# Optimization experiments

Measured on AMD Instinct MI355X. Metric: run time of the kernel, lower is better.

The kernel has to match this reference:

```python
import jax, jax.numpy as jnp
import numpy as np

B, N, D = 4, 2048, 1024


def setup_inputs() -> dict:
    key = jax.random.key(0)
    ks = jax.random.split(key, 9)
    x = jax.random.normal(ks[0], (B, N, D), dtype=jnp.float32)
    # causal mask: True = masked (set to -inf), per dot_product_attention semantics
    mask = jnp.triu(jnp.ones((N, N), dtype=bool), k=1)
    mask = jnp.broadcast_to(mask, (B, N, N))
    scale = 1.0 / np.sqrt(D)
    Wq = jax.random.normal(ks[1], (D, D), dtype=jnp.float32) * scale
    Wk = jax.random.normal(ks[2], (D, D), dtype=jnp.float32) * scale
    Wv = jax.random.normal(ks[3], (D, D), dtype=jnp.float32) * scale
    Wo = jax.random.normal(ks[4], (D, D), dtype=jnp.float32) * scale
    bq = jnp.zeros((D,), dtype=jnp.float32)
    bk = jnp.zeros((D,), dtype=jnp.float32)
    bv = jnp.zeros((D,), dtype=jnp.float32)
    bo = jnp.zeros((D,), dtype=jnp.float32)
    return {"x": x, "mask": mask, "Wq": Wq, "bq": bq, "Wk": Wk, "bk": bk,
            "Wv": Wv, "bv": bv, "Wo": Wo, "bo": bo}


def reference(x, mask, Wq, bq, Wk, bk, Wv, bv, Wo, bo):
    # QKV projections (single-head despite docstring; module never splits heads)
    Q = x @ Wq + bq  # [b, n, d]
    K = x @ Wk + bk
    V = x @ Wv + bv
    d = K.shape[-1]
    scores = jnp.einsum('bqd,bkd->bqk', Q, K) / jnp.sqrt(jnp.asarray(d, Q.dtype))
    min_infty = jnp.finfo(scores.dtype).min
    scores = jnp.where(mask, min_infty, scores)
    weights = jax.nn.softmax(scores, axis=-1)
    attention = jnp.einsum('bqk,bkd->bqd', weights, V)
    out = attention @ Wo + bo
    return out
```

## Files before the change

### kernel.cpp

```cpp
#include <hip/hip_runtime.h>
#include <hip/hip_bf16.h>

typedef __attribute__((ext_vector_type(8))) short short8;
typedef __attribute__((ext_vector_type(4))) float f32x4;

__device__ inline float b2f(unsigned short u) {
    union { unsigned int i; float f; } c; c.i = ((unsigned int)u) << 16; return c.f;
}
__device__ inline unsigned short f2b(float f) {
    __hip_bfloat16 h = __float2bfloat16(f);
    return *reinterpret_cast<unsigned short*>(&h);
}

__device__ inline void gl_lds16(const unsigned short* g, unsigned short* ldsbase) {
    __builtin_amdgcn_global_load_lds(
        (const __attribute__((address_space(1))) unsigned int*)(g),
        (__attribute__((address_space(3))) unsigned int*)(ldsbase),
        16, 0, 0);
}

__global__ __launch_bounds__(256) void cvt_f32_bf16(
    const float* __restrict__ src, unsigned short* __restrict__ dst, int n4)
{
    int i = blockIdx.x * 256 + threadIdx.x;
    if (i >= n4) return;
    float4 v = ((const float4*)src)[i];
    union { unsigned short u[4]; unsigned long long ll; } p;
    p.u[0] = f2b(v.x); p.u[1] = f2b(v.y); p.u[2] = f2b(v.z); p.u[3] = f2b(v.w);
    ((unsigned long long*)dst)[i] = p.ll;
}

__global__ __launch_bounds__(256) void cvt_weights4(
    const float* __restrict__ s0, const float* __restrict__ s1, const float* __restrict__ s2,
    const float* __restrict__ s3,
    unsigned short* __restrict__ d0, unsigned short* __restrict__ d1,
    unsigned short* __restrict__ d2, unsigned short* __restrict__ d3)
{
    const int z = blockIdx.z;
    if (z == 3) {
        const int i = (blockIdx.y * 32 + blockIdx.x) * 256 + threadIdx.x;
        float4 v = ((const float4*)s3)[i];
        union { unsigned short u[4]; unsigned long long ll; } p;
        p.u[0] = f2b(v.x); p.u[1] = f2b(v.y); p.u[2] = f2b(v.z); p.u[3] = f2b(v.w);
        ((unsigned long long*)d3)[i] = p.ll;
        return;
    }
    const float* src = z == 0 ? s0 : z == 1 ? s1 : s2;
    unsigned short* dst = z == 0 ? d0 : z == 1 ? d1 : d2;
    __shared__ float tile[32][33];
    const int c0 = blockIdx.x * 32, r0 = blockIdx.y * 32;
    const int tx = threadIdx.x & 31, ty = threadIdx.x >> 5;
    #pragma unroll
    for (int i = ty; i < 32; i += 8)
        tile[i][tx] = src[(long)(r0 + i) * 1024 + c0 + tx];
    __syncthreads();
    #pragma unroll
    for (int i = ty; i < 32; i += 8)
        dst[(long)(c0 + i) * 1024 + r0 + tx] = f2b(tile[tx][i]);
}

__global__ __launch_bounds__(64) void make_bvo(
    const unsigned short* __restrict__ Wot, const float* __restrict__ bv,
    const float* __restrict__ bo, float* __restrict__ bvo)
{
    const int n = blockIdx.x;
    const int lane = threadIdx.x;
    const unsigned short* row = Wot + (long)n * 1024;
    float acc = 0.f;
    #pragma unroll
    for (int pass = 0; pass < 2; pass++) {
        const int k = pass * 512 + lane * 8;
        short8 wv = *(const short8*)(row + k);
        #pragma unroll
        for (int j = 0; j < 8; j++)
            acc += bv[k + j] * b2f((unsigned short)wv[j]);
    }
    #pragma unroll
    for (int off = 32; off > 0; off >>= 1) acc += __shfl_xor(acc, off, 64);
    if (lane == 0) bvo[n] = acc + bo[n];
}

#define TILE_DECLS \
    __shared__ __attribute__((aligned(16))) unsigned short As[2 * 128 * 32]; \
    __shared__ __attribute__((aligned(16))) unsigned short Bs[2 * 128 * 32]; \
    const int t = threadIdx.x, lane = t & 63, w = t >> 6; \
    const int wr = w >> 1, wc = w & 1; \
    const int lrow = lane & 15, quad = lane >> 4; \
    f32x4 acc[4][4]; \
    _Pragma("unroll") for (int i = 0; i < 4; i++) \
        _Pragma("unroll") for (int j = 0; j < 4; j++) \
            acc[i][j] = (f32x4){0.f, 0.f, 0.f, 0.f};

#define TILE_KLOOP(gA, lda, gB, ldb, Keff) \
    for (int k0 = 0; k0 < (Keff); k0 += 64) { \
        _Pragma("unroll") for (int p = 0; p < 2; p++) \
            _Pragma("unroll") for (int h = 0; h < 2; h++) { \
                gl_lds16((gA) + (long)h * 16 * (lda) + k0 + p * 32, \
                         &As[p * 4096 + (w * 32 + h * 16) * 32]); \
                gl_lds16((gB) + (long)h * 16 * (ldb) + k0 + p * 32, \
                         &Bs[p * 4096 + (w * 32 + h * 16) * 32]); \
            } \
        __syncthreads(); \
        _Pragma("unroll") for (int p = 0; p < 2; p++) { \
            short8 af[4], bfr[4]; \
            _Pragma("unroll") for (int mi = 0; mi < 4; mi++) \
                af[mi] = *(const short8*)&As[p * 4096 + (wr * 64 + mi * 16 + lrow) * 32 + quad * 8]; \
            _Pragma("unroll") for (int ni = 0; ni < 4; ni++) \
                bfr[ni] = *(const short8*)&Bs[p * 4096 + (wc * 64 + ni * 16 + lrow) * 32 + quad * 8]; \
            _Pragma("unroll") for (int mi = 0; mi < 4; mi++) \
                _Pragma("unroll") for (int ni = 0; ni < 4; ni++) \
                    acc[mi][ni] = __builtin_amdgcn_mfma_f32_16x16x32_bf16( \
                        af[mi], bfr[ni], acc[mi][ni], 0, 0, 0); \
        } \
        __syncthreads(); \
    }

__global__ __launch_bounds__(256) void qkv_proj(
    const unsigned short* __restrict__ A,
    const unsigned short* __restrict__ Wqt, const unsigned short* __restrict__ Wkt,
    const unsigned short* __restrict__ Wvot,
    const float* __restrict__ bq, const float* __restrict__ bk,
    unsigned short* __restrict__ Q, unsigned short* __restrict__ Km,
    unsigned short* __restrict__ Vot)
{
    const int bm = blockIdx.x, bn = blockIdx.y;
    const int r = bn >> 3, bnn = bn & 7;
    const unsigned short* Bt = (r == 0) ? Wqt : (r == 1) ? Wkt : Wvot;
    const float* bias = (r == 0) ? bq : (r == 1) ? bk : nullptr;
    const int m0 = bm * 128, n0 = bnn * 128;

    TILE_DECLS

    const unsigned short* gA = A  + (long)(m0 + w * 32 + (lane >> 2)) * 1024 + (lane & 3) * 8;
    const unsigned short* gB = Bt + (long)(n0 + w * 32 + (lane >> 2)) * 1024 + (lane & 3) * 8;
    TILE_KLOOP(gA, 1024, gB, 1024, 1024)

    #pragma unroll
    for (int mi = 0; mi < 4; mi++) {
        const int m = m0 + wr * 64 + mi * 16 + quad * 4;
        #pragma unroll
        for (int ni = 0; ni < 4; ni++) {
            const int n = n0 + wc * 64 + ni * 16 + lrow;
            const float bvl = bias ? bias[n] : 0.f;
            if (r < 2) {
                unsigned short* out = (r == 0) ? Q : Km;
                #pragma unroll
                for (int rg = 0; rg < 4; rg++)
                    out[(long)(m + rg) * 1024 + n] = f2b(acc[mi][ni][rg] + bvl);
            } else {
                #pragma unroll
                for (int rg = 0; rg < 4; rg++)
                    Vot[(long)n * 8192 + m + rg] = f2b(acc[mi][ni][rg]);
            }
        }
    }
}

template<bool CAUSAL2, bool KCAUSAL, int OMODE>
__global__ __launch_bounds__(256) void gemm64(
    const unsigned short* __restrict__ A, const unsigned short* __restrict__ Bt,
    const float* __restrict__ bias, void* __restrict__ Cv,
    int K, int lda, int ldb, int ldc, long sA, long sB, long sC, float scale)
{
    const int bm = KCAUSAL ? (gridDim.x - 1 - blockIdx.x) : blockIdx.x;
    const int bn = blockIdx.y, bz = blockIdx.z;
    if (CAUSAL2 && bm < 2 * bn) return;
    A  += (long)bz * sA;
    Bt += (long)bz * sB;
    const int m0 = bm * 64, n0 = bn * 128;

    __shared__ __attribute__((aligned(16))) unsigned short As[2 * 64 * 32];
    __shared__ __attribute__((aligned(16))) unsigned short Bs[2 * 128 * 32];

    const int t = threadIdx.x, lane = t & 63, w = t >> 6;
    const int wr = w >> 1, wc = w & 1;
    const int lrow = lane & 15, quad = lane >> 4;

    f32x4 acc[2][4];
    #pragma unroll
    for (int i = 0; i < 2; i++)
        #pragma unroll
        for (int j = 0; j < 4; j++)
            acc[i][j] = (f32x4){0.f, 0.f, 0.f, 0.f};

    const int KeffRaw = KCAUSAL ? ((bm >> 1) + 1) * 128 : K;
    const int Keff = KeffRaw < K ? KeffRaw : K;

    const unsigned short* gA = A  + (long)(m0 + w * 16 + (lane >> 2)) * lda + (lane & 3) * 8;
    const unsigned short* gB = Bt + (long)(n0 + w * 32 + (lane >> 2)) * ldb + (lane & 3) * 8;

    for (int k0 = 0; k0 < Keff; k0 += 64) {
        #pragma unroll
        for (int p = 0; p < 2; p++) {
            gl_lds16(gA + k0 + p * 32, &As[p * 2048 + (w * 16) * 32]);
            gl_lds16(gB + k0 + p * 32, &Bs[p * 4096 + (w * 32) * 32]);
            gl_lds16(gB + (long)16 * ldb + k0 + p * 32, &Bs[p * 4096 + (w * 32 + 16) * 32]);
        }
        __syncthreads();
        #pragma unroll
        for (int p = 0; p < 2; p++) {
            short8 af[2], bfr[4];
            #pragma unroll
            for (int mi = 0; mi < 2; mi++)
                af[mi] = *(const short8*)&As[p * 2048 + (wr * 32 + mi * 16 + lrow) * 32 + quad * 8];
            #pragma unroll
            for (int ni = 0; ni < 4; ni++)
                bfr[ni] = *(const short8*)&Bs[p * 4096 + (wc * 64 + ni * 16 + lrow) * 32 + quad * 8];
            #pragma unroll
            for (int mi = 0; mi < 2; mi++)
                #pragma unroll
                for (int ni = 0; ni < 4; ni++)
                    acc[mi][ni] = __builtin_amdgcn_mfma_f32_16x16x32_bf16(
                        af[mi], bfr[ni], acc[mi][ni], 0, 0, 0);
        }
        __syncthreads();
    }

    #pragma unroll
    for (int mi = 0; mi < 2; mi++) {
        const int m = m0 + wr * 32 + mi * 16 + quad * 4;
        #pragma unroll
        for (int ni = 0; ni < 4; ni++) {
            const int n = n0 + wc * 64 + ni * 16 + lrow;
            const float bvl = bias ? bias[n] : 0.f;
            #pragma unroll
            for (int rg = 0; rg < 4; rg++) {
                const float val = acc[mi][ni][rg] * scale + bvl;
                if (OMODE == 1)
                    ((float*)Cv)[(long)bz * sC + (long)(m + rg) * ldc + n] = val;
                else
                    ((unsigned short*)Cv)[(long)bz * sC + (long)(m + rg) * ldc + n] = f2b(val);
            }
        }
    }
}

__global__ __launch_bounds__(256) void softmax_causal(unsigned short* __restrict__ S)
{
    const long row = blockIdx.x;
    const int i = (int)(row & 2047);
    unsigned short* base = S + row * 2048;
    const int t = threadIdx.x;
    const int padded = ((i >> 7) + 1) << 7;
    const int j0 = t * 8;
    const bool active = j0 < padded;

    __shared__ float red[4];

    float v[8];
    if (active) {
        short8 s8 = *(const short8*)(base + j0);
        #pragma unroll
        for (int jj = 0; jj < 8; jj++)
            v[jj] = (j0 + jj <= i) ? b2f((unsigned short)s8[jj]) : -3.0e38f;
    } else {
        #pragma unroll
        for (int jj = 0; jj < 8; jj++) v[jj] = -3.0e38f;
    }

    float lmax = v[0];
    #pragma unroll
    for (int jj = 1; jj < 8; jj++) lmax = fmaxf(lmax, v[jj]);
    #pragma unroll
    for (int off = 32; off > 0; off >>= 1) lmax = fmaxf(lmax, __shfl_xor(lmax, off, 64));
    if ((t & 63) == 0) red[t >> 6] = lmax;
    __syncthreads();
    const float gmax = fmaxf(fmaxf(red[0], red[1]), fmaxf(red[2], red[3]));
    __syncthreads();

    float lsum = 0.f;
    #pragma unroll
    for (int jj = 0; jj < 8; jj++) {
        v[jj] = (v[jj] > -1.0e37f) ? __expf(v[jj] - gmax) : 0.f;
        lsum += v[jj];
    }
    #pragma unroll
    for (int off = 32; off > 0; off >>= 1) lsum += __shfl_xor(lsum, off, 64);
    if ((t & 63) == 0) red[t >> 6] = lsum;
    __syncthreads();
    const float inv = 1.0f / (red[0] + red[1] + red[2] + red[3]);

    if (active) {
        short8 p8;
        #pragma unroll
        for (int jj = 0; jj < 8; jj++) p8[jj] = (short)f2b(v[jj] * inv);
        *(short8*)(base + j0) = p8;
    }
}

extern "C" void kernel_launch(void* const* d_in, const int* in_sizes, int n_in,
                              void* d_out, int out_size, void* d_ws, size_t ws_size,
                              hipStream_t stream)
{
    const float* x  = (const float*)d_in[0];
    const float* Wq = (const float*)d_in[2];
    const float* bq = (const float*)d_in[3];
    const float* Wk = (const float*)d_in[4];
    const float* bk = (const float*)d_in[5];
    const float* Wv = (const float*)d_in[6];
    const float* bv = (const float*)d_in[7];
    const float* Wo = (const float*)d_in[8];
    const float* bo = (const float*)d_in[9];

    unsigned short* ws = (unsigned short*)d_ws;
    const long XSZ = 8192L * 1024;
    const long WSZ = 1024L * 1024;
    unsigned short* xb   = ws;
    unsigned short* Wqt  = ws + XSZ;
    unsigned short* Wkt  = Wqt + WSZ;
    unsigned short* Wot  = Wkt + WSZ;
    unsigned short* Wvb  = Wot + WSZ;
    unsigned short* Wvot = Wvb + WSZ;
    unsigned short* Q    = Wvot + WSZ;
    unsigned short* Km   = Q + XSZ;
    unsigned short* Vot  = Km + XSZ;
    unsigned short* S    = Vot + XSZ;
    float*          bvo  = (float*)(S + 4L * 2048 * 2048);

    const dim3 blk(256);

    cvt_f32_bf16<<<dim3(8192), blk, 0, stream>>>(x, xb, (int)(XSZ / 4));
    cvt_weights4<<<dim3(32, 32, 4), blk, 0, stream>>>(
        Wq, Wk, Wo, Wv, Wqt, Wkt, Wot, Wvb);
    make_bvo    <<<dim3(1024), dim3(64), 0, stream>>>(Wot, bv, bo, bvo);

    gemm64<false, false, 0><<<dim3(16, 8, 1), blk, 0, stream>>>(
        Wot, Wvb, nullptr, Wvot, 1024, 1024, 1024, 1024, 0, 0, 0, 1.f);

    qkv_proj<<<dim3(64, 24), blk, 0, stream>>>(
        xb, Wqt, Wkt, Wvot, bq, bk, Q, Km, Vot);

    gemm64<true, false, 0><<<dim3(32, 16, 4), blk, 0, stream>>>(
        Q, Km, nullptr, S, 1024, 1024, 1024, 2048,
        2048L * 1024, 2048L * 1024, 2048L * 2048, 0.03125f);

    softmax_causal<<<dim3(4 * 2048), blk, 0, stream>>>(S);

    gemm64<false, true, 1><<<dim3(32, 8, 4), blk, 0, stream>>>(
        S, Vot, bvo, (float*)d_out, 2048, 2048, 8192, 1024,
        2048L * 2048, 2048, 2048L * 1024, 1.f);
}
```

Baseline: 347.6 us.

## Merge prep kernels, fuse causal QK^T with last-block softmax, retile PV to 128x128

```diff
diff --git a/kernel.cpp b/kernel.cpp
--- a/kernel.cpp
+++ b/kernel.cpp
@@ -19,65 +19,54 @@
         16, 0, 0);
 }
 
-__global__ __launch_bounds__(256) void cvt_f32_bf16(
-    const float* __restrict__ src, unsigned short* __restrict__ dst, int n4)
-{
-    int i = blockIdx.x * 256 + threadIdx.x;
-    if (i >= n4) return;
-    float4 v = ((const float4*)src)[i];
-    union { unsigned short u[4]; unsigned long long ll; } p;
-    p.u[0] = f2b(v.x); p.u[1] = f2b(v.y); p.u[2] = f2b(v.z); p.u[3] = f2b(v.w);
-    ((unsigned long long*)dst)[i] = p.ll;
-}
-
-__global__ __launch_bounds__(256) void cvt_weights4(
-    const float* __restrict__ s0, const float* __restrict__ s1, const float* __restrict__ s2,
-    const float* __restrict__ s3,
-    unsigned short* __restrict__ d0, unsigned short* __restrict__ d1,
-    unsigned short* __restrict__ d2, unsigned short* __restrict__ d3)
-{
-    const int z = blockIdx.z;
-    if (z == 3) {
-        const int i = (blockIdx.y * 32 + blockIdx.x) * 256 + threadIdx.x;
-        float4 v = ((const float4*)s3)[i];
-        union { unsigned short u[4]; unsigned long long ll; } p;
-        p.u[0] = f2b(v.x); p.u[1] = f2b(v.y); p.u[2] = f2b(v.z); p.u[3] = f2b(v.w);
-        ((unsigned long long*)d3)[i] = p.ll;
-        return;
-    }
-    const float* src = z == 0 ? s0 : z == 1 ? s1 : s2;
-    unsigned short* dst = z == 0 ? d0 : z == 1 ? d1 : d2;
-    __shared__ float tile[32][33];
-    const int c0 = blockIdx.x * 32, r0 = blockIdx.y * 32;
-    const int tx = threadIdx.x & 31, ty = threadIdx.x >> 5;
-    #pragma unroll
-    for (int i = ty; i < 32; i += 8)
-        tile[i][tx] = src[(long)(r0 + i) * 1024 + c0 + tx];
-    __syncthreads();
-    #pragma unroll
-    for (int i = ty; i < 32; i += 8)
-        dst[(long)(c0 + i) * 1024 + r0 + tx] = f2b(tile[tx][i]);
-}
-
-__global__ __launch_bounds__(64) void make_bvo(
-    const unsigned short* __restrict__ Wot, const float* __restrict__ bv,
-    const float* __restrict__ bo, float* __restrict__ bvo)
-{
-    const int n = blockIdx.x;
-    const int lane = threadIdx.x;
-    const unsigned short* row = Wot + (long)n * 1024;
-    float acc = 0.f;
-    #pragma unroll
-    for (int pass = 0; pass < 2; pass++) {
-        const int k = pass * 512 + lane * 8;
-        short8 wv = *(const short8*)(row + k);
-        #pragma unroll
-        for (int j = 0; j < 8; j++)
-            acc += bv[k + j] * b2f((unsigned short)wv[j]);
-    }
-    #pragma unroll
-    for (int off = 32; off > 0; off >>= 1) acc += __shfl_xor(acc, off, 64);
-    if (lane == 0) bvo[n] = acc + bo[n];
+__global__ __launch_bounds__(256) void prep(
+    const float* __restrict__ x, const float* __restrict__ Wq,
+    const float* __restrict__ Wk, const float* __restrict__ Wv,
+    const float* __restrict__ Wo, const float* __restrict__ bv,
+    const float* __restrict__ bo,
+    unsigned short* __restrict__ xb, unsigned short* __restrict__ Wqt,
+    unsigned short* __restrict__ Wkt, unsigned short* __restrict__ Wot,
+    unsigned short* __restrict__ Wvb, float* __restrict__ bvo,
+    unsigned int* __restrict__ tick)
+{
+    const int bid = blockIdx.x, nb = gridDim.x, t = threadIdx.x;
+    __shared__ float tile[32 * 33];
+
+    for (int j = bid; j < 3072; j += nb) {
+        const float* src = (j < 1024) ? Wq : (j < 2048) ? Wk : Wo;
+        unsigned short* dst = (j < 1024) ? Wqt : (j < 2048) ? Wkt : Wot;
+        const int ji = j & 1023;
+        const int c0 = (ji & 31) * 32, r0 = (ji >> 5) * 32;
+        const int tx = t & 31, ty = t >> 5;
+        #pragma unroll
+        for (int i2 = ty; i2 < 32; i2 += 8)
+            tile[i2 * 33 + tx] = src[(long)(r0 + i2) * 1024 + c0 + tx];
+        __syncthreads();
+        #pragma unroll
+        for (int i2 = ty; i2 < 32; i2 += 8)
+            dst[(long)(c0 + i2) * 1024 + r0 + tx] = f2b(tile[tx * 33 + i2]);
+        __syncthreads();
+    }
+    for (long i = (long)bid * 256 + t; i < 2097152; i += (long)nb * 256) {
+        float4 v = ((const float4*)x)[i];
+        union { unsigned short u[4]; unsigned long long ll; } pk;
+        pk.u[0] = f2b(v.x); pk.u[1] = f2b(v.y); pk.u[2] = f2b(v.z); pk.u[3] = f2b(v.w);
+        ((unsigned long long*)xb)[i] = pk.ll;
+    }
+    for (long i = (long)bid * 256 + t; i < 262144; i += (long)nb * 256) {
+        float4 v = ((const float4*)Wv)[i];
+        union { unsigned short u[4]; unsigned long long ll; } pk;
+        pk.u[0] = f2b(v.x); pk.u[1] = f2b(v.y); pk.u[2] = f2b(v.z); pk.u[3] = f2b(v.w);
+        ((unsigned long long*)Wvb)[i] = pk.ll;
+    }
+    if (bid >= 3072 && bid < 3076) {
+        const int n = (bid - 3072) * 256 + t;
+        float acc = bo[n];
+        #pragma unroll 8
+        for (int k = 0; k < 1024; k++) acc += bv[k] * Wo[(long)k * 1024 + n];
+        bvo[n] = acc;
+    }
+    if (bid == nb - 1 && t < 64) tick[t] = 0u;
 }
 
 #define TILE_DECLS \
@@ -156,69 +145,112 @@
     }
 }
 
-template<bool CAUSAL2, bool KCAUSAL, int OMODE>
-__global__ __launch_bounds__(256) void gemm64(
+__global__ __launch_bounds__(256) void qk_softmax(
+    const unsigned short* __restrict__ Q, const unsigned short* __restrict__ Km,
+    unsigned short* __restrict__ S, unsigned int* __restrict__ tick)
+{
+    const int qidx = 135 - (int)blockIdx.x;
+    int bm = (int)((sqrtf(8.f * qidx + 1.f) - 1.f) * 0.5f);
+    while ((bm + 1) * (bm + 2) / 2 <= qidx) bm++;
+    while (bm * (bm + 1) / 2 > qidx) bm--;
+    const int bn = qidx - bm * (bm + 1) / 2;
+    const int bz = blockIdx.y;
+
+    const unsigned short* A  = Q  + (long)bz * 2048 * 1024;
+    const unsigned short* Bt = Km + (long)bz * 2048 * 1024;
+    unsigned short* Sb = S + (long)bz * 2048 * 2048;
+    const int m0 = bm * 128, n0 = bn * 128;
+
+    __shared__ int sdone;
+    TILE_DECLS
+
+    const unsigned short* gA = A  + (long)(m0 + w * 32 + (lane >> 2)) * 1024 + (lane & 3) * 8;
+    const unsigned short* gB = Bt + (long)(n0 + w * 32 + (lane >> 2)) * 1024 + (lane & 3) * 8;
+    TILE_KLOOP(gA, 1024, gB, 1024, 1024)
+
+    #pragma unroll
+    for (int mi = 0; mi < 4; mi++) {
+        const int m = m0 + wr * 64 + mi * 16 + quad * 4;
+        #pragma unroll
+        for (int ni = 0; ni < 4; ni++) {
+            const int n = n0 + wc * 64 + ni * 16 + lrow;
+            #pragma unroll
+            for (int rg = 0; rg < 4; rg++)
+                Sb[(long)(m + rg) * 2048 + n] = f2b(acc[mi][ni][rg] * 0.03125f);
+        }
+    }
+
+    __threadfence();
+    __syncthreads();
+    if (t == 0) {
+        unsigned int old = __hip_atomic_fetch_add(&tick[bz * 16 + bm], 1u,
+                               __ATOMIC_ACQ_REL, __HIP_MEMORY_SCOPE_AGENT);
+        sdone = (old == (unsigned)bm) ? 1 : 0;
+    }
+    __syncthreads();
+    if (!sdone) return;
+    __threadfence();
+
+    const int cols = (bm + 1) * 128;
+    for (int r = w; r < 128; r += 4) {
+        const int i = m0 + r;
+        unsigned short* base = Sb + (long)i * 2048;
+        const int len = i + 1;
+        float mx = -3.0e38f;
+        for (int c = lane * 8; c < cols; c += 512) {
+            short8 v = *(const short8*)(base + c);
+            #pragma unroll
+            for (int j = 0; j < 8; j++)
+                if (c + j < len) mx = fmaxf(mx, b2f((unsigned short)v[j]));
+        }
+        #pragma unroll
+        for (int off = 32; off > 0; off >>= 1) mx = fmaxf(mx, __shfl_xor(mx, off, 64));
+        float sum = 0.f;
+        for (int c = lane * 8; c < cols; c += 512) {
+            short8 v = *(const short8*)(base + c);
+            #pragma unroll
+            for (int j = 0; j < 8; j++)
+                if (c + j < len) sum += __expf(b2f((unsigned short)v[j]) - mx);
+        }
+        #pragma unroll
+        for (int off = 32; off > 0; off >>= 1) sum += __shfl_xor(sum, off, 64);
+        const float inv = 1.0f / sum;
+        for (int c = lane * 8; c < cols; c += 512) {
+            short8 v = *(const short8*)(base + c);
+            short8 o;
+            #pragma unroll
+            for (int j = 0; j < 8; j++)
+                o[j] = (c + j < len)
+                    ? (short)f2b(__expf(b2f((unsigned short)v[j]) - mx) * inv)
+                    : (short)0;
+            *(short8*)(base + c) = o;
+        }
+    }
+}
+
+template<bool KCAUSAL, int OMODE>
+__global__ __launch_bounds__(256) void gemm128(
     const unsigned short* __restrict__ A, const unsigned short* __restrict__ Bt,
     const float* __restrict__ bias, void* __restrict__ Cv,
     int K, int lda, int ldb, int ldc, long sA, long sB, long sC, float scale)
 {
     const int bm = KCAUSAL ? (gridDim.x - 1 - blockIdx.x) : blockIdx.x;
     const int bn = blockIdx.y, bz = blockIdx.z;
-    if (CAUSAL2 && bm < 2 * bn) return;
     A  += (long)bz * sA;
     Bt += (long)bz * sB;
-    const int m0 = bm * 64, n0 = bn * 128;
-
-    __shared__ __attribute__((aligned(16))) unsigned short As[2 * 64 * 32];
-    __shared__ __attribute__((aligned(16))) unsigned short Bs[2 * 128 * 32];
-
-    const int t = threadIdx.x, lane = t & 63, w = t >> 6;
-    const int wr = w >> 1, wc = w & 1;
-    const int lrow = lane & 15, quad = lane >> 4;
-
-    f32x4 acc[2][4];
-    #pragma unroll
-    for (int i = 0; i < 2; i++)
-        #pragma unroll
-        for (int j = 0; j < 4; j++)
-            acc[i][j] = (f32x4){0.f, 0.f, 0.f, 0.f};
-
-    const int KeffRaw = KCAUSAL ? ((bm >> 1) + 1) * 128 : K;
+    const int m0 = bm * 128, n0 = bn * 128;
+
+    TILE_DECLS
+
+    const int KeffRaw = KCAUSAL ? (bm + 1) * 128 : K;
     const int Keff = KeffRaw < K ? KeffRaw : K;
-
-    const unsigned short* gA = A  + (long)(m0 + w * 16 + (lane >> 2)) * lda + (lane & 3) * 8;
+    const unsigned short* gA = A  + (long)(m0 + w * 32 + (lane >> 2)) * lda + (lane & 3) * 8;
     const unsigned short* gB = Bt + (long)(n0 + w * 32 + (lane >> 2)) * ldb + (lane & 3) * 8;
-
-    for (int k0 = 0; k0 < Keff; k0 += 64) {
-        #pragma unroll
-        for (int p = 0; p < 2; p++) {
-            gl_lds16(gA + k0 + p * 32, &As[p * 2048 + (w * 16) * 32]);
-            gl_lds16(gB + k0 + p * 32, &Bs[p * 4096 + (w * 32) * 32]);
-            gl_lds16(gB + (long)16 * ldb + k0 + p * 32, &Bs[p * 4096 + (w * 32 + 16) * 32]);
-        }
-        __syncthreads();
-        #pragma unroll
-        for (int p = 0; p < 2; p++) {
-            short8 af[2], bfr[4];
-            #pragma unroll
-            for (int mi = 0; mi < 2; mi++)
-                af[mi] = *(const short8*)&As[p * 2048 + (wr * 32 + mi * 16 + lrow) * 32 + quad * 8];
-            #pragma unroll
-            for (int ni = 0; ni < 4; ni++)
-                bfr[ni] = *(const short8*)&Bs[p * 4096 + (wc * 64 + ni * 16 + lrow) * 32 + quad * 8];
-            #pragma unroll
-            for (int mi = 0; mi < 2; mi++)
-                #pragma unroll
-                for (int ni = 0; ni < 4; ni++)
-                    acc[mi][ni] = __builtin_amdgcn_mfma_f32_16x16x32_bf16(
-                        af[mi], bfr[ni], acc[mi][ni], 0, 0, 0);
-        }
-        __syncthreads();
-    }
-
-    #pragma unroll
-    for (int mi = 0; mi < 2; mi++) {
-        const int m = m0 + wr * 32 + mi * 16 + quad * 4;
+    TILE_KLOOP(gA, lda, gB, ldb, Keff)
+
+    #pragma unroll
+    for (int mi = 0; mi < 4; mi++) {
+        const int m = m0 + wr * 64 + mi * 16 + quad * 4;
         #pragma unroll
         for (int ni = 0; ni < 4; ni++) {
             const int n = n0 + wc * 64 + ni * 16 + lrow;
@@ -235,56 +267,66 @@
     }
 }
 
-__global__ __launch_bounds__(256) void softmax_causal(unsigned short* __restrict__ S)
-{
-    const long row = blockIdx.x;
-    const int i = (int)(row & 2047);
-    unsigned short* base = S + row * 2048;
-    const int t = threadIdx.x;
-    const int padded = ((i >> 7) + 1) << 7;
-    const int j0 = t * 8;
-    const bool active = j0 < padded;
-
-    __shared__ float red[4];
-
-    float v[8];
-    if (active) {
-        short8 s8 = *(const short8*)(base + j0);
-        #pragma unroll
-        for (int jj = 0; jj < 8; jj++)
-            v[jj] = (j0 + jj <= i) ? b2f((unsigned short)s8[jj]) : -3.0e38f;
-    } else {
-        #pragma unroll
-        for (int jj = 0; jj < 8; jj++) v[jj] = -3.0e38f;
-    }
-
-    float lmax = v[0];
-    #pragma unroll
-    for (int jj = 1; jj < 8; jj++) lmax = fmaxf(lmax, v[jj]);
-    #pragma unroll
-    for (int off = 32; off > 0; off >>= 1) lmax = fmaxf(lmax, __shfl_xor(lmax, off, 64));
-    if ((t & 63) == 0) red[t >> 6] = lmax;
-    __syncthreads();
-    const float gmax = fmaxf(fmaxf(red[0], red[1]), fmaxf(red[2], red[3]));
-    __syncthreads();
-
-    float lsum = 0.f;
-    #pragma unroll
-    for (int jj = 0; jj < 8; jj++) {
-        v[jj] = (v[jj] > -1.0e37f) ? __expf(v[jj] - gmax) : 0.f;
-        lsum += v[jj];
-    }
-    #pragma unroll
-    for (int off = 32; off > 0; off >>= 1) lsum += __shfl_xor(lsum, off, 64);
-    if ((t & 63) == 0) red[t >> 6] = lsum;
-    __syncthreads();
-    const float inv = 1.0f / (red[0] + red[1] + red[2] + red[3]);
-
-    if (active) {
-        short8 p8;
-        #pragma unroll
-        for (int jj = 0; jj < 8; jj++) p8[jj] = (short)f2b(v[jj] * inv);
-        *(short8*)(base + j0) = p8;
+__global__ __launch_bounds__(256) void gemm64w(
+    const unsigned short* __restrict__ A, const unsigned short* __restrict__ Bt,
+    unsigned short* __restrict__ C)
+{
+    const int m0 = blockIdx.x * 64, n0 = blockIdx.y * 128;
+
+    __shared__ __attribute__((aligned(16))) unsigned short As[2 * 64 * 32];
+    __shared__ __attribute__((aligned(16))) unsigned short Bs[2 * 128 * 32];
+
+    const int t = threadIdx.x, lane = t & 63, w = t >> 6;
+    const int wr = w >> 1, wc = w & 1;
+    const int lrow = lane & 15, quad = lane >> 4;
+
+    f32x4 acc[2][4];
+    #pragma unroll
+    for (int i = 0; i < 2; i++)
+        #pragma unroll
+        for (int j = 0; j < 4; j++)
+            acc[i][j] = (f32x4){0.f, 0.f, 0.f, 0.f};
+
+    const unsigned short* gA = A  + (long)(m0 + w * 16 + (lane >> 2)) * 1024 + (lane & 3) * 8;
+    const unsigned short* gB = Bt + (long)(n0 + w * 32 + (lane >> 2)) * 1024 + (lane & 3) * 8;
+
+    for (int k0 = 0; k0 < 1024; k0 += 64) {
+        #pragma unroll
+        for (int p = 0; p < 2; p++) {
+            gl_lds16(gA + k0 + p * 32, &As[p * 2048 + (w * 16) * 32]);
+            gl_lds16(gB + k0 + p * 32, &Bs[p * 4096 + (w * 32) * 32]);
+            gl_lds16(gB + (long)16 * 1024 + k0 + p * 32, &Bs[p * 4096 + (w * 32 + 16) * 32]);
+        }
+        __syncthreads();
+        #pragma unroll
+        for (int p = 0; p < 2; p++) {
+            short8 af[2], bfr[4];
+            #pragma unroll
+            for (int mi = 0; mi < 2; mi++)
+                af[mi] = *(const short8*)&As[p * 2048 + (wr * 32 + mi * 16 + lrow) * 32 + quad * 8];
+            #pragma unroll
+            for (int ni = 0; ni < 4; ni++)
+                bfr[ni] = *(const short8*)&Bs[p * 4096 + (wc * 64 + ni * 16 + lrow) * 32 + quad * 8];
+            #pragma unroll
+            for (int mi = 0; mi < 2; mi++)
+                #pragma unroll
+                for (int ni = 0; ni < 4; ni++)
+                    acc[mi][ni] = __builtin_amdgcn_mfma_f32_16x16x32_bf16(
+                        af[mi], bfr[ni], acc[mi][ni], 0, 0, 0);
+        }
+        __syncthreads();
+    }
+
+    #pragma unroll
+    for (int mi = 0; mi < 2; mi++) {
+        const int m = m0 + wr * 32 + mi * 16 + quad * 4;
+        #pragma unroll
+        for (int ni = 0; ni < 4; ni++) {
+            const int n = n0 + wc * 64 + ni * 16 + lrow;
+            #pragma unroll
+            for (int rg = 0; rg < 4; rg++)
+                C[(long)(m + rg) * 1024 + n] = f2b(acc[mi][ni][rg]);
+        }
     }
 }
 
@@ -316,27 +358,21 @@
     unsigned short* Vot  = Km + XSZ;
     unsigned short* S    = Vot + XSZ;
     float*          bvo  = (float*)(S + 4L * 2048 * 2048);
+    unsigned int*   tick = (unsigned int*)(bvo + 1024);
 
     const dim3 blk(256);
 
-    cvt_f32_bf16<<<dim3(8192), blk, 0, stream>>>(x, xb, (int)(XSZ / 4));
-    cvt_weights4<<<dim3(32, 32, 4), blk, 0, stream>>>(
-        Wq, Wk, Wo, Wv, Wqt, Wkt, Wot, Wvb);
-    make_bvo    <<<dim3(1024), dim3(64), 0, stream>>>(Wot, bv, bo, bvo);
-
-    gemm64<false, false, 0><<<dim3(16, 8, 1), blk, 0, stream>>>(
-        Wot, Wvb, nullptr, Wvot, 1024, 1024, 1024, 1024, 0, 0, 0, 1.f);
+    prep<<<dim3(4096), blk, 0, stream>>>(
+        x, Wq, Wk, Wv, Wo, bv, bo, xb, Wqt, Wkt, Wot, Wvb, bvo, tick);
+
+    gemm64w<<<dim3(16, 8), blk, 0, stream>>>(Wot, Wvb, Wvot);
 
     qkv_proj<<<dim3(64, 24), blk, 0, stream>>>(
         xb, Wqt, Wkt, Wvot, bq, bk, Q, Km, Vot);
 
-    gemm64<true, false, 0><<<dim3(32, 16, 4), blk, 0, stream>>>(
-        Q, Km, nullptr, S, 1024, 1024, 1024, 2048,
-        2048L * 1024, 2048L * 1024, 2048L * 2048, 0.03125f);
-
-    softmax_causal<<<dim3(4 * 2048), blk, 0, stream>>>(S);
-
-    gemm64<false, true, 1><<<dim3(32, 8, 4), blk, 0, stream>>>(
+    qk_softmax<<<dim3(136, 4), blk, 0, stream>>>(Q, Km, S, tick);
+
+    gemm128<true, 1><<<dim3(16, 8, 4), blk, 0, stream>>>(
         S, Vot, bvo, (float*)d_out, 2048, 2048, 8192, 1024,
         2048L * 2048, 2048, 2048L * 1024, 1.f);
 }
```

New measurement: 633.9 us. +82.4%, slower.
